# Kernel tuning notes

Hardware: AMD Instinct MI355X
Metric: run time of the kernel (lower is better)

The kernel has to match this reference:

```python
import jax, jax.numpy as jnp
import numpy as np

B, C, H, W = 8, 3, 1024, 1024
N, D, PS, NB, NH = 512, 256, 16, 8, 4


def _bin_matrix():
    # static radial-binning averaging matrix for a PS x (PS//2+1) rfft2 spectrum
    h, w = PS, PS // 2 + 1
    fy = np.fft.fftfreq(h)
    fx = np.linspace(0.0, 0.5, w)
    r = np.sqrt(fx[None, :] ** 2 + fy[:, None] ** 2)
    max_r = r.max() + 1e-6
    edges = np.linspace(0.0, max_r, NB + 1)
    idx = np.clip(np.searchsorted(edges, r.ravel(), side='right') - 1, 0, NB - 1)
    M = np.zeros((NB, h * w), np.float32)
    M[idx, np.arange(h * w)] = 1.0
    cnt = M.sum(1, keepdims=True)
    return M / np.maximum(cnt, 1.0)

_BIN_M = jnp.asarray(_bin_matrix())


def _ln(x, g, b, eps=1e-5):
    m = x.mean(-1, keepdims=True)
    v = x.var(-1, keepdims=True)
    return g * (x - m) / jnp.sqrt(v + eps) + b


def _gelu(x):
    return jax.nn.gelu(x, approximate=False)


def setup_inputs() -> dict:
    key = jax.random.key(0)
    ks = jax.random.split(key, 16)
    xav = lambda k, o, i: (jax.random.normal(k, (o, i)) / np.sqrt(i)).astype(jnp.float32)
    z = lambda n: jnp.zeros((n,), jnp.float32)
    o1 = lambda n: jnp.ones((n,), jnp.float32)
    FD = 2 * NB
    return {
        'image': jax.random.normal(ks[0], (B, C, H, W), jnp.float32),
        'point_coords': jax.random.uniform(ks[1], (B, N, 2), jnp.float32, 0.0, float(W)),
        'point_labels': jax.random.randint(ks[2], (B, N), 0, 2),
        'pe_w': xav(ks[3], D, D), 'pe_b': z(D),
        'type_emb': (0.02 * jax.random.normal(ks[4], (2, D))).astype(jnp.float32),
        'fbi': (1.0 + 0.1 * jax.random.normal(ks[5], (NB,))).astype(jnp.float32),
        'fe1_w': xav(ks[6], D // 2, FD), 'fe1_b': z(D // 2),
        'feln1_g': o1(D // 2), 'feln1_b': z(D // 2),
        'fe2_w': xav(ks[7], D, D // 2), 'fe2_b': z(D),
        'feln2_g': o1(D), 'feln2_b': z(D),
        'in_w': xav(ks[8], 3 * D, D), 'in_b': z(3 * D),
        'ao_w': xav(ks[9], D, D), 'ao_b': z(D),
        'n1_g': o1(D), 'n1_b': z(D),
        'f1_w': xav(ks[10], 2 * D, D), 'f1_b': z(2 * D),
        'f2_w': xav(ks[11], D, 2 * D), 'f2_b': z(D),
        'n2_g': o1(D), 'n2_b': z(D),
        'op_w': xav(ks[12], D, D), 'op_b': z(D),
    }


def reference(image, point_coords, point_labels, pe_w, pe_b, type_emb, fbi,
              fe1_w, fe1_b, feln1_g, feln1_b, fe2_w, fe2_b, feln2_g, feln2_b,
              in_w, in_b, ao_w, ao_b, n1_g, n1_b, f1_w, f1_b, f2_w, f2_b,
              n2_g, n2_b, op_w, op_b):
    Bv, Cv, Hv, Wv = image.shape
    Nv = point_coords.shape[1]
    # --- sinusoidal positional encoding (SAM style) + linear proj ---
    nc = point_coords / jnp.array([Wv, Hv], jnp.float32)
    dim_t = 10000.0 ** (2.0 * jnp.arange(D // 4, dtype=jnp.float32) / (D // 4))
    ax = (nc[..., 0:1] * (2.0 * np.pi)) / dim_t          # [B,N,D/4]
    ay = (nc[..., 1:2] * (2.0 * np.pi)) / dim_t
    pe = jnp.concatenate([jnp.sin(ax), jnp.cos(ax), jnp.sin(ay), jnp.cos(ay)], -1)
    spatial = pe @ pe_w.T + pe_b + type_emb[point_labels]  # [B,N,D]
    # --- batched per-point patch gather + rfft2 + radial binning ---
    gray = image.mean(1)                                   # [B,H,W]
    pc = jax.lax.stop_gradient(point_coords)               # .long() detaches in torch
    half = PS // 2
    px = jnp.clip(pc[..., 0].astype(jnp.int32), half, Wv - half - 1)
    py = jnp.clip(pc[..., 1].astype(jnp.int32), half, Hv - half - 1)
    off = jnp.arange(PS) - half
    rows = py[..., None] + off                             # [B,N,PS]
    cols = px[..., None] + off
    bidx = jnp.arange(Bv)[:, None, None, None]
    patches = gray[bidx, rows[..., :, None], cols[..., None, :]]  # [B,N,PS,PS]
    fft = jnp.fft.rfft2(patches, norm='ortho')             # [B,N,PS,PS//2+1]
    mag_bins = jnp.abs(fft).reshape(Bv, Nv, -1) @ _BIN_M.T    # [B,N,NB]
    ph_bins = jnp.angle(fft).reshape(Bv, Nv, -1) @ _BIN_M.T
    feat = jnp.concatenate([mag_bins * jax.nn.softmax(fbi), ph_bins], -1)  # [B,N,2*NB]
    # --- freq encoder MLP ---
    h1 = _gelu(_ln(feat @ fe1_w.T + fe1_b, feln1_g, feln1_b))
    freq = _ln(h1 @ fe2_w.T + fe2_b, feln2_g, feln2_b)     # [B,N,D]
    # --- cross-attention fusion (spatial = Q, freq = K/V) ---
    hd = D // NH
    q = (spatial @ in_w[:D].T + in_b[:D]).reshape(Bv, Nv, NH, hd)
    k = (freq @ in_w[D:2 * D].T + in_b[D:2 * D]).reshape(Bv, Nv, NH, hd)
    v = (freq @ in_w[2 * D:].T + in_b[2 * D:]).reshape(Bv, Nv, NH, hd)
    att = jax.nn.softmax(jnp.einsum('bqhd,bkhd->bhqk', q, k) / np.sqrt(hd), -1)
    o = jnp.einsum('bhqk,bkhd->bqhd', att, v).reshape(Bv, Nv, D)
    x = _ln(spatial + (o @ ao_w.T + ao_b), n1_g, n1_b)
    ffn = _gelu(x @ f1_w.T + f1_b) @ f2_w.T + f2_b
    x = _ln(x + ffn, n2_g, n2_b)
    return x @ op_w.T + op_b
```

## Files before the change

kernel.cpp:

```cpp
#include <hip/hip_runtime.h>
#include <math.h>


typedef __attribute__((ext_vector_type(8))) short short8;
typedef __attribute__((ext_vector_type(4))) float floatx4;
typedef unsigned short u16;
typedef unsigned long long u64;

__device__ __forceinline__ float gelu_f(float x) {
  return 0.5f * x * (1.0f + erff(x * 0.70710678118654752f));
}

__device__ __forceinline__ u16 bf16_rn(float x) {
  union { float f; unsigned u; } v; v.f = x;
  unsigned r = v.u + 0x7fffu + ((v.u >> 16) & 1u);
  return (u16)(r >> 16);
}

__device__ __forceinline__ void split_bf16(float x, u16& h, u16& l) {
  h = bf16_rn(x);
  union { unsigned u; float f; } hv; hv.u = ((unsigned)h) << 16;
  l = bf16_rn(x - hv.f);
}

#define W_PE   0
#define W_FE1  65536
#define W_FE2  67584
#define W_IN   100352
#define W_AO   296960
#define W_F1   362496
#define W_F2   493568
#define W_OP   624640


template <int NA, int K>
__device__ __forceinline__ void mm16_swz(
    const u16* Ah, const u16* Al, const int S,
    const u16* __restrict__ Bh, const u16* __restrict__ Bl,
    floatx4* acc)
{
  const int t = threadIdx.x;
  const int w = t >> 6, lane = t & 63;
  const int lm = lane & 15, kg = lane >> 4;
  #pragma unroll
  for (int it = 0; it < K / 32; ++it) {
    const short8 a_h = *(const short8*)&Ah[lm * S + it * 32 + kg * 8];
    const short8 a_l = *(const short8*)&Al[lm * S + it * 32 + kg * 8];
    #pragma unroll
    for (int nj = 0; nj < NA; nj++) {
      const size_t wo = (size_t)(((w * NA + nj) * (K / 32) + it) * 512 + lane * 8);
      const short8 b_h = *(const short8*)&Bh[wo];
      const short8 b_l = *(const short8*)&Bl[wo];
      acc[nj] = __builtin_amdgcn_mfma_f32_16x16x32_bf16(a_h, b_h, acc[nj], 0, 0, 0);
      acc[nj] = __builtin_amdgcn_mfma_f32_16x16x32_bf16(a_h, b_l, acc[nj], 0, 0, 0);
      acc[nj] = __builtin_amdgcn_mfma_f32_16x16x32_bf16(a_l, b_h, acc[nj], 0, 0, 0);
    }
  }
}

__device__ __forceinline__ void stage16(
    const u16* __restrict__ Gh, const u16* __restrict__ Gl,
    u16* Lh, u16* Ll)
{
  const int t = threadIdx.x;
  #pragma unroll
  for (int i = 0; i < 2; i++) {
    const int s = t + i * 256;
    const int row = s >> 5, c = (s & 31) * 8;
    *(short8*)&Lh[row * 264 + c] = *(const short8*)&Gh[(size_t)row * 256 + c];
    *(short8*)&Ll[row * 264 + c] = *(const short8*)&Gl[(size_t)row * 256 + c];
  }
  __syncthreads();
}

template <int N_, int NA>
__device__ __forceinline__ void ln_rows(const float (&v)[NA][4], float* red1, float* red2,
                                        float (&mean)[4], float (&rstd)[4])
{
  const int t = threadIdx.x;
  const int w = t >> 6;
  const int lane = t & 63;
  const int kg = lane >> 4;
  float s1[4] = {0.f,0.f,0.f,0.f}, s2[4] = {0.f,0.f,0.f,0.f};
  #pragma unroll
  for (int nj = 0; nj < NA; nj++)
    #pragma unroll
    for (int r = 0; r < 4; r++) { s1[r] += v[nj][r]; s2[r] += v[nj][r] * v[nj][r]; }
  #pragma unroll
  for (int r = 0; r < 4; r++) {
    #pragma unroll
    for (int off = 1; off < 16; off <<= 1) {
      s1[r] += __shfl_xor(s1[r], off);
      s2[r] += __shfl_xor(s2[r], off);
    }
  }
  __syncthreads();
  if ((lane & 15) == 0) {
    #pragma unroll
    for (int r = 0; r < 4; r++) {
      red1[w * 16 + kg * 4 + r] = s1[r];
      red2[w * 16 + kg * 4 + r] = s2[r];
    }
  }
  __syncthreads();
  #pragma unroll
  for (int r = 0; r < 4; r++) {
    const int rw = kg * 4 + r;
    const float a = red1[rw] + red1[16 + rw] + red1[32 + rw] + red1[48 + rw];
    const float b = red2[rw] + red2[16 + rw] + red2[32 + rw] + red2[48 + rw];
    mean[r] = a * (1.0f / N_);
    rstd[r] = rsqrtf(b * (1.0f / N_) - mean[r] * mean[r] + 1e-5f);
  }
}

__device__ __forceinline__ void store_swz(
    u16* __restrict__ Wh, u16* __restrict__ Wl, const int segbase,
    const int rel, const int kshift, const float4 v)
{
  const int K = 1 << kshift;
  const int n = rel >> kshift;
  const int k = rel & (K - 1);
  const int off8 = ((n >> 4) * (K >> 5) + (k >> 5)) * 512
                 + (((k >> 3) & 3) * 16 + (n & 15)) * 8 + (k & 7);
  u16 h0,h1,h2,h3,l0,l1,l2,l3;
  split_bf16(v.x,h0,l0); split_bf16(v.y,h1,l1);
  split_bf16(v.z,h2,l2); split_bf16(v.w,h3,l3);
  *(u64*)&Wh[segbase + off8] = (u64)h0 | ((u64)h1<<16) | ((u64)h2<<32) | ((u64)h3<<48);
  *(u64*)&Wl[segbase + off8] = (u64)l0 | ((u64)l1<<16) | ((u64)l2<<32) | ((u64)l3<<48);
}

__global__ __launch_bounds__(64) void k0_prep(
    const float* __restrict__ image, const float* __restrict__ coords,
    const float* __restrict__ fbi,
    const float* __restrict__ pe_w, const float* __restrict__ fe1_w,
    const float* __restrict__ fe2_w, const float* __restrict__ in_w,
    const float* __restrict__ ao_w, const float* __restrict__ f1_w,
    const float* __restrict__ f2_w, const float* __restrict__ op_w,
    u16* __restrict__ Wh, u16* __restrict__ Wl,
    u16* __restrict__ PEh, u16* __restrict__ PEl,
    u16* __restrict__ FEATh, u16* __restrict__ FEATl)
{
  const int blk = blockIdx.x;
  const int lane = threadIdx.x;

  if (blk < 2696) {
    const int idx = (blk * 64 + lane) * 4;
    if (idx < W_FE1) {
      store_swz(Wh, Wl, W_PE, idx - W_PE, 8, *(const float4*)&pe_w[idx - W_PE]);
    } else if (idx < W_FE2) {
      const int rel = idx - W_FE1;
      const float4 v = *(const float4*)&fe1_w[rel];
      u16 h0,h1,h2,h3,l0,l1,l2,l3;
      split_bf16(v.x,h0,l0); split_bf16(v.y,h1,l1);
      split_bf16(v.z,h2,l2); split_bf16(v.w,h3,l3);
      *(u64*)&Wh[idx] = (u64)h0 | ((u64)h1<<16) | ((u64)h2<<32) | ((u64)h3<<48);
      *(u64*)&Wl[idx] = (u64)l0 | ((u64)l1<<16) | ((u64)l2<<32) | ((u64)l3<<48);
    } else if (idx < W_IN) {
      store_swz(Wh, Wl, W_FE2, idx - W_FE2, 7, *(const float4*)&fe2_w[idx - W_FE2]);
    } else if (idx < W_AO) {
      store_swz(Wh, Wl, W_IN, idx - W_IN, 8, *(const float4*)&in_w[idx - W_IN]);
    } else if (idx < W_F1) {
      store_swz(Wh, Wl, W_AO, idx - W_AO, 8, *(const float4*)&ao_w[idx - W_AO]);
    } else if (idx < W_F2) {
      store_swz(Wh, Wl, W_F1, idx - W_F1, 8, *(const float4*)&f1_w[idx - W_F1]);
    } else if (idx < W_OP) {
      store_swz(Wh, Wl, W_F2, idx - W_F2, 9, *(const float4*)&f2_w[idx - W_F2]);
    } else {
      store_swz(Wh, Wl, W_OP, idx - W_OP, 8, *(const float4*)&op_w[idx - W_OP]);
    }
    return;
  }

  const int id = blk - 2696;
  const int b  = id >> 9;
  const float pcx = coords[id * 2 + 0];
  const float pcy = coords[id * 2 + 1];

  {
    const float TWO_PI = 6.283185307179586f;
    const float dimt = expf((float)lane * 0.28782313662425572f);
    const float ax = (pcx * (1.0f / 1024.0f)) * TWO_PI / dimt;
    const float ay = (pcy * (1.0f / 1024.0f)) * TWO_PI / dimt;
    u16 h, l;
    split_bf16(sinf(ax), h, l); PEh[id*256+lane]     = h; PEl[id*256+lane]     = l;
    split_bf16(cosf(ax), h, l); PEh[id*256+lane+64]  = h; PEl[id*256+lane+64]  = l;
    split_bf16(sinf(ay), h, l); PEh[id*256+lane+128] = h; PEl[id*256+lane+128] = l;
    split_bf16(cosf(ay), h, l); PEh[id*256+lane+192] = h; PEl[id*256+lane+192] = l;
  }

  int px = (int)pcx; px = px < 8 ? 8 : (px > 1015 ? 1015 : px);
  int py = (int)pcy; py = py < 8 ? 8 : (py > 1015 ? 1015 : py);

  __shared__ float patch[256];
  __shared__ float ct[16], st[16];
  __shared__ float Gre[144], Gim[144];
  __shared__ float msum[8], psum[8];
  __shared__ int cnt8[8];
  {
    const float* img = image + (size_t)b * 3145728;
    #pragma unroll
    for (int i = 0; i < 4; i++) {
      const int p = i * 64 + lane;
      const int r = p >> 4, c = p & 15;
      const int off = (py - 8 + r) * 1024 + (px - 8 + c);
      const float s = img[off] + img[off + 1048576] + img[off + 2097152];
      patch[r * 16 + c] = s * (1.0f / 3.0f);
    }
  }
  if (lane < 16) {
    float c, s;
    if ((lane & 3) == 0) {
      const float cv[4] = {1.0f, 0.0f, -1.0f, 0.0f};
      const float sv[4] = {0.0f, -1.0f, 0.0f, 1.0f};
      c = cv[lane >> 2]; s = sv[lane >> 2];
    } else {
      const float a = -3.14159265358979f * (float)lane * 0.125f;
      c = cosf(a); s = sinf(a);
    }
    ct[lane] = c; st[lane] = s;
  }
  if (lane < 8) { msum[lane] = 0.0f; psum[lane] = 0.0f; cnt8[lane] = 0; }
  __syncthreads();

  for (int tt = lane; tt < 144; tt += 64) {
    const int y = tt / 9, kx = tt - y * 9;
    float re = 0.0f, im = 0.0f;
    #pragma unroll
    for (int x = 0; x < 16; x++) {
      const int w = (x * kx) & 15;
      const float pv = patch[y * 16 + x];
      re = fmaf(pv, ct[w], re);
      im = fmaf(pv, st[w], im);
    }
    Gre[tt] = re; Gim[tt] = im;
  }
  __syncthreads();

  for (int tt = lane; tt < 144; tt += 64) {
    const int ky = tt / 9, kx = tt - ky * 9;
    float re = 0.0f, im = 0.0f;
    #pragma unroll
    for (int y = 0; y < 16; y++) {
      const int w = (y * ky) & 15;
      const float gr = Gre[y * 9 + kx], gi = Gim[y * 9 + kx];
      re = fmaf(gr, ct[w], re);
      re = fmaf(-gi, st[w], re);
      im = fmaf(gr, st[w], im);
      im = fmaf(gi, ct[w], im);
    }
    if (((ky & 7) == 0) && ((kx & 7) == 0)) im = 0.0f;
    const float mag = sqrtf(re * re + im * im) * 0.0625f;
    const float ph  = atan2f(im, re);

    const float fy = (ky < 8) ? (float)ky * 0.0625f : (float)(ky - 16) * 0.0625f;
    const float fx = (float)kx * 0.0625f;
    const float r = sqrtf(fx * fx + fy * fy);
    const float max_r = 0.7071077811865476f;
    const float stepf = max_r * 0.125f;
    int idx = 0;
    #pragma unroll
    for (int kq = 1; kq <= 8; kq++) {
      const float e = (kq == 8) ? max_r : stepf * (float)kq;
      if (r >= e) idx = kq;
    }
    if (idx > 7) idx = 7;
    atomicAdd(&msum[idx], mag);
    atomicAdd(&psum[idx], ph);
    atomicAdd(&cnt8[idx], 1);
  }
  __syncthreads();

  if (lane < 8) {
    float fm = fbi[0];
    #pragma unroll
    for (int j = 1; j < 8; j++) fm = fmaxf(fm, fbi[j]);
    float se = 0.0f;
    #pragma unroll
    for (int j = 0; j < 8; j++) se += expf(fbi[j] - fm);
    const float smx = expf(fbi[lane] - fm) / se;
    const float c = (float)(cnt8[lane] > 0 ? cnt8[lane] : 1);
    u16 h, l;
    split_bf16((msum[lane] / c) * smx, h, l);
    FEATh[id*16+lane] = h; FEATl[id*16+lane] = l;
    split_bf16(psum[lane] / c, h, l);
    FEATh[id*16+8+lane] = h; FEATl[id*16+8+lane] = l;
  }
}

__global__ __launch_bounds__(256) void k1_front(
    const u16* __restrict__ Wh, const u16* __restrict__ Wl,
    const u16* __restrict__ PEh, const u16* __restrict__ PEl,
    const u16* __restrict__ FEATh, const u16* __restrict__ FEATl,
    const float* __restrict__ pe_b, const int* __restrict__ labels,
    const float* __restrict__ temb,
    const float* __restrict__ fe1_b, const float* __restrict__ feln1_g, const float* __restrict__ feln1_b,
    const float* __restrict__ fe2_b, const float* __restrict__ feln2_g, const float* __restrict__ feln2_b,
    float* __restrict__ SPATIAL32, u16* __restrict__ SPh, u16* __restrict__ SPl,
    u16* __restrict__ FQh, u16* __restrict__ FQl)
{
  __shared__ __align__(16) u16 smem[8448];
  __shared__ float redbuf[128];
  const int blk = blockIdx.x;
  const int t = threadIdx.x;
  const int w = t >> 6, lane = t & 63;
  const int lm = lane & 15, kg = lane >> 4;

  if (blk < 256) {
    const int m0 = blk * 16;
    u16* Lh = smem;
    u16* Ll = smem + 4224;
    stage16(PEh + (size_t)m0 * 256, PEl + (size_t)m0 * 256, Lh, Ll);
    floatx4 acc[4];
    #pragma unroll
    for (int j = 0; j < 4; j++) acc[j] = (floatx4){0.f,0.f,0.f,0.f};
    mm16_swz<4, 256>(Lh, Ll, 264, Wh + W_PE, Wl + W_PE, acc);
    #pragma unroll
    for (int nj = 0; nj < 4; nj++) {
      const int col = w * 64 + nj * 16 + lm;
      #pragma unroll
      for (int r = 0; r < 4; r++) {
        const int row = m0 + kg * 4 + r;
        const float v = acc[nj][r] + pe_b[col] + temb[labels[row] * 256 + col];
        SPATIAL32[(size_t)row * 256 + col] = v;
        u16 h, l; split_bf16(v, h, l);
        SPh[(size_t)row * 256 + col] = h;
        SPl[(size_t)row * 256 + col] = l;
      }
    }
    return;
  }

  const int m0 = (blk - 256) * 16;
  u16* h1h = smem;
  u16* h1l = smem + 2176;

  floatx4 acc1[2];
  acc1[0] = (floatx4){0.f,0.f,0.f,0.f};
  acc1[1] = (floatx4){0.f,0.f,0.f,0.f};
  {
    const short8 zz = {0,0,0,0,0,0,0,0};
    const short8 a_h = (kg < 2) ? *(const short8*)&FEATh[(size_t)(m0 + lm) * 16 + kg * 8] : zz;
    const short8 a_l = (kg < 2) ? *(const short8*)&FEATl[(size_t)(m0 + lm) * 16 + kg * 8] : zz;
    #pragma unroll
    for (int nj = 0; nj < 2; nj++) {
      const int col = w * 32 + nj * 16 + lm;
      const short8 b_h = (kg < 2) ? *(const short8*)&Wh[W_FE1 + (size_t)col * 16 + kg * 8] : zz;
      const short8 b_l = (kg < 2) ? *(const short8*)&Wl[W_FE1 + (size_t)col * 16 + kg * 8] : zz;
      acc1[nj] = __builtin_amdgcn_mfma_f32_16x16x32_bf16(a_h, b_h, acc1[nj], 0, 0, 0);
      acc1[nj] = __builtin_amdgcn_mfma_f32_16x16x32_bf16(a_h, b_l, acc1[nj], 0, 0, 0);
      acc1[nj] = __builtin_amdgcn_mfma_f32_16x16x32_bf16(a_l, b_h, acc1[nj], 0, 0, 0);
    }
  }

  float v1[2][4];
  #pragma unroll
  for (int nj = 0; nj < 2; nj++) {
    const int col = w * 32 + nj * 16 + lm;
    #pragma unroll
    for (int r = 0; r < 4; r++) v1[nj][r] = acc1[nj][r] + fe1_b[col];
  }
  float mean[4], rstd[4];
  ln_rows<128, 2>(v1, redbuf, redbuf + 64, mean, rstd);
  #pragma unroll
  for (int nj = 0; nj < 2; nj++) {
    const int col = w * 32 + nj * 16 + lm;
    #pragma unroll
    for (int r = 0; r < 4; r++) {
      float y = feln1_g[col] * (v1[nj][r] - mean[r]) * rstd[r] + feln1_b[col];
      y = gelu_f(y);
      u16 h, l; split_bf16(y, h, l);
      h1h[(kg * 4 + r) * 136 + col] = h;
      h1l[(kg * 4 + r) * 136 + col] = l;
    }
  }
  __syncthreads();

  floatx4 acc2[4];
  #pragma unroll
  for (int j = 0; j < 4; j++) acc2[j] = (floatx4){0.f,0.f,0.f,0.f};
  mm16_swz<4, 128>(h1h, h1l, 136, Wh + W_FE2, Wl + W_FE2, acc2);

  float v2[4][4];
  #pragma unroll
  for (int nj = 0; nj < 4; nj++) {
    const int col = w * 64 + nj * 16 + lm;
    #pragma unroll
    for (int r = 0; r < 4; r++) v2[nj][r] = acc2[nj][r] + fe2_b[col];
  }
  ln_rows<256, 4>(v2, redbuf, redbuf + 64, mean, rstd);
  #pragma unroll
  for (int nj = 0; nj < 4; nj++) {
    const int col = w * 64 + nj * 16 + lm;
    #pragma unroll
    for (int r = 0; r < 4; r++) {
      const int rw = m0 + kg * 4 + r;
      float y = feln2_g[col] * (v2[nj][r] - mean[r]) * rstd[r] + feln2_b[col];
      u16 h, l; split_bf16(y, h, l);
      FQh[(size_t)rw * 256 + col] = h;
      FQl[(size_t)rw * 256 + col] = l;
    }
  }
}

__global__ __launch_bounds__(256) void k2_qkv(
    const u16* __restrict__ Wh, const u16* __restrict__ Wl,
    const u16* __restrict__ SPh, const u16* __restrict__ SPl,
    const u16* __restrict__ FQh, const u16* __restrict__ FQl,
    const float* __restrict__ in_b,
    u16* __restrict__ Qh, u16* __restrict__ Ql,
    u16* __restrict__ Kh, u16* __restrict__ Kl,
    u16* __restrict__ Vth, u16* __restrict__ Vtl)
{
  __shared__ __align__(16) u16 smem[8448];
  const int bx = blockIdx.x;
  const int seg = bx >> 8;
  const int m0 = (bx & 255) * 16;
  const int t = threadIdx.x;
  const int w = t >> 6, lane = t & 63;
  const int lm = lane & 15, kg = lane >> 4;

  const u16 *Ah, *Al; const u16 *Wsh, *Wsl; const float* bias;
  if (seg == 0)      { Ah = SPh; Al = SPl; Wsh = Wh + W_IN;          Wsl = Wl + W_IN;          bias = in_b; }
  else if (seg == 1) { Ah = FQh; Al = FQl; Wsh = Wh + W_IN + 65536;  Wsl = Wl + W_IN + 65536;  bias = in_b + 256; }
  else               { Ah = FQh; Al = FQl; Wsh = Wh + W_IN + 131072; Wsl = Wl + W_IN + 131072; bias = in_b + 512; }

  u16* Lh = smem;
  u16* Ll = smem + 4224;
  stage16(Ah + (size_t)m0 * 256, Al + (size_t)m0 * 256, Lh, Ll);

  floatx4 acc[4];
  #pragma unroll
  for (int j = 0; j < 4; j++) acc[j] = (floatx4){0.f,0.f,0.f,0.f};
  mm16_swz<4, 256>(Lh, Ll, 264, Wsh, Wsl, acc);

  if (seg < 2) {
    u16* oh = (seg == 0) ? Qh : Kh;
    u16* ol = (seg == 0) ? Ql : Kl;
    #pragma unroll
    for (int nj = 0; nj < 4; nj++) {
      const int col = w * 64 + nj * 16 + lm;
      #pragma unroll
      for (int r = 0; r < 4; r++) {
        const int row = m0 + kg * 4 + r;
        u16 h, l; split_bf16(acc[nj][r] + bias[col], h, l);
        oh[(size_t)row * 256 + col] = h;
        ol[(size_t)row * 256 + col] = l;
      }
    }
  } else {
    #pragma unroll
    for (int nj = 0; nj < 4; nj++) {
      const int col = w * 64 + nj * 16 + lm;
      u64 hp = 0, lp = 0;
      #pragma unroll
      for (int r = 0; r < 4; r++) {
        u16 h, l; split_bf16(acc[nj][r] + bias[col], h, l);
        hp |= ((u64)h) << (16 * r);
        lp |= ((u64)l) << (16 * r);
      }
      *(u64*)&Vth[(size_t)col * 4096 + m0 + kg * 4] = hp;
      *(u64*)&Vtl[(size_t)col * 4096 + m0 + kg * 4] = lp;
    }
  }
}

__global__ __launch_bounds__(256) void k3_attn(
    const u16* __restrict__ Qh, const u16* __restrict__ Ql,
    const u16* __restrict__ Kh, const u16* __restrict__ Kl,
    const u16* __restrict__ Vth, const u16* __restrict__ Vtl,
    u16* __restrict__ Oh, u16* __restrict__ Ol)
{
  __shared__ __align__(16) u16 smem[36864];
  u16* sQh = smem;
  u16* sQl = smem + 4608;
  u16* sKh = smem + 9216;
  u16* sKl = smem + 13824;
  u16* sVh = smem + 18432;
  u16* sVl = smem + 23040;
  u16* sPh = smem + 27648;
  u16* sPl = smem + 32256;

  const int qt = blockIdx.x & 7;
  const int bh = blockIdx.x >> 3;
  const int b = bh >> 2, h = bh & 3;
  const int t = threadIdx.x;
  const int w = t >> 6, lane = t & 63;
  const int lm = lane & 15, kg = lane >> 4;
  const int qrow0 = b * 512 + qt * 64;

  #pragma unroll
  for (int i = 0; i < 2; i++) {
    const int s = t + i * 256;
    const int r = s >> 3, d = (s & 7) * 8;
    *(short8*)&sQh[r * 72 + d] = *(const short8*)&Qh[(size_t)(qrow0 + r) * 256 + h * 64 + d];
    *(short8*)&sQl[r * 72 + d] = *(const short8*)&Ql[(size_t)(qrow0 + r) * 256 + h * 64 + d];
  }

  float m_i[4], l_i[4];
  floatx4 o_acc[4];
  #pragma unroll
  for (int r = 0; r < 4; r++) { m_i[r] = -INFINITY; l_i[r] = 0.0f; }
  #pragma unroll
  for (int dj = 0; dj < 4; dj++) o_acc[dj] = (floatx4){0.f, 0.f, 0.f, 0.f};

  __syncthreads();
  short8 q_h[2], q_l[2];
  #pragma unroll
  for (int ks = 0; ks < 2; ks++) {
    const int off = (w * 16 + lm) * 72 + ks * 32 + kg * 8;
    q_h[ks] = *(const short8*)&sQh[off];
    q_l[ks] = *(const short8*)&sQl[off];
  }

  for (int kt = 0; kt < 8; kt++) {
    __syncthreads();
    {
      const int krow0 = b * 512 + kt * 64;
      #pragma unroll
      for (int i = 0; i < 2; i++) {
        const int s = t + i * 256;
        const int r = s >> 3, d = (s & 7) * 8;
        *(short8*)&sKh[r * 72 + d] = *(const short8*)&Kh[(size_t)(krow0 + r) * 256 + h * 64 + d];
        *(short8*)&sKl[r * 72 + d] = *(const short8*)&Kl[(size_t)(krow0 + r) * 256 + h * 64 + d];
        *(short8*)&sVh[r * 72 + d] = *(const short8*)&Vth[(size_t)(h * 64 + r) * 4096 + krow0 + d];
        *(short8*)&sVl[r * 72 + d] = *(const short8*)&Vtl[(size_t)(h * 64 + r) * 4096 + krow0 + d];
      }
    }
    __syncthreads();

    floatx4 sacc[4];
    #pragma unroll
    for (int nj = 0; nj < 4; nj++) sacc[nj] = (floatx4){0.f, 0.f, 0.f, 0.f};
    #pragma unroll
    for (int ks = 0; ks < 2; ks++) {
      #pragma unroll
      for (int nj = 0; nj < 4; nj++) {
        const int off = (nj * 16 + lm) * 72 + ks * 32 + kg * 8;
        const short8 kb_h = *(const short8*)&sKh[off];
        const short8 kb_l = *(const short8*)&sKl[off];
        sacc[nj] = __builtin_amdgcn_mfma_f32_16x16x32_bf16(q_h[ks], kb_h, sacc[nj], 0, 0, 0);
        sacc[nj] = __builtin_amdgcn_mfma_f32_16x16x32_bf16(q_h[ks], kb_l, sacc[nj], 0, 0, 0);
        sacc[nj] = __builtin_amdgcn_mfma_f32_16x16x32_bf16(q_l[ks], kb_h, sacc[nj], 0, 0, 0);
      }
    }

    float pp[4][4];
    #pragma unroll
    for (int r = 0; r < 4; r++) {
      float mx = -INFINITY;
      #pragma unroll
      for (int nj = 0; nj < 4; nj++) {
        sacc[nj][r] *= 0.125f;
        mx = fmaxf(mx, sacc[nj][r]);
      }
      #pragma unroll
      for (int off = 1; off < 16; off <<= 1) mx = fmaxf(mx, __shfl_xor(mx, off));
      const float mnew = fmaxf(m_i[r], mx);
      const float alpha = expf(m_i[r] - mnew);
      m_i[r] = mnew;
      float rs = 0.0f;
      #pragma unroll
      for (int nj = 0; nj < 4; nj++) { pp[nj][r] = expf(sacc[nj][r] - mnew); rs += pp[nj][r]; }
      #pragma unroll
      for (int off = 1; off < 16; off <<= 1) rs += __shfl_xor(rs, off);
      l_i[r] = l_i[r] * alpha + rs;
      #pragma unroll
      for (int dj = 0; dj < 4; dj++) o_acc[dj][r] *= alpha;
    }

    #pragma unroll
    for (int nj = 0; nj < 4; nj++)
      #pragma unroll
      for (int r = 0; r < 4; r++) {
        u16 ph, pl; split_bf16(pp[nj][r], ph, pl);
        sPh[(w * 16 + kg * 4 + r) * 72 + nj * 16 + lm] = ph;
        sPl[(w * 16 + kg * 4 + r) * 72 + nj * 16 + lm] = pl;
      }

    #pragma unroll
    for (int ks = 0; ks < 2; ks++) {
      const short8 p_h = *(const short8*)&sPh[(w * 16 + lm) * 72 + ks * 32 + kg * 8];
      const short8 p_l = *(const short8*)&sPl[(w * 16 + lm) * 72 + ks * 32 + kg * 8];
      #pragma unroll
      for (int dj = 0; dj < 4; dj++) {
        const int off = (dj * 16 + lm) * 72 + ks * 32 + kg * 8;
        const short8 v_h = *(const short8*)&sVh[off];
        const short8 v_l = *(const short8*)&sVl[off];
        o_acc[dj] = __builtin_amdgcn_mfma_f32_16x16x32_bf16(p_h, v_h, o_acc[dj], 0, 0, 0);
        o_acc[dj] = __builtin_amdgcn_mfma_f32_16x16x32_bf16(p_l, v_h, o_acc[dj], 0, 0, 0);
        o_acc[dj] = __builtin_amdgcn_mfma_f32_16x16x32_bf16(p_h, v_l, o_acc[dj], 0, 0, 0);
      }
    }
  }

  #pragma unroll
  for (int r = 0; r < 4; r++) {
    const float inv_l = 1.0f / l_i[r];
    const size_t rowoff = (size_t)(qrow0 + w * 16 + kg * 4 + r) * 256 + h * 64;
    #pragma unroll
    for (int dj = 0; dj < 4; dj++) {
      u16 oh, ol; split_bf16(o_acc[dj][r] * inv_l, oh, ol);
      Oh[rowoff + dj * 16 + lm] = oh;
      Ol[rowoff + dj * 16 + lm] = ol;
    }
  }
}

__global__ __launch_bounds__(256) void k4_tail(
    const u16* __restrict__ Wh, const u16* __restrict__ Wl,
    const u16* __restrict__ Oh, const u16* __restrict__ Ol,
    const float* __restrict__ SPATIAL32,
    const float* __restrict__ ao_b, const float* __restrict__ n1_g, const float* __restrict__ n1_b,
    const float* __restrict__ f1_b, const float* __restrict__ f2_b,
    const float* __restrict__ n2_g, const float* __restrict__ n2_b,
    const float* __restrict__ op_b, float* __restrict__ OUT)
{
  __shared__ __align__(16) u16 smem[25088];
  __shared__ float redbuf[128];
  u16* B1h = smem;
  u16* B1l = smem + 4224;
  u16* Fh  = smem + 8448;
  u16* Fl  = smem + 16768;

  const int t = threadIdx.x;
  const int w = t >> 6, lane = t & 63;
  const int lm = lane & 15, kg = lane >> 4;
  const int m0 = blockIdx.x * 16;

  stage16(Oh + (size_t)m0 * 256, Ol + (size_t)m0 * 256, B1h, B1l);
  floatx4 acc[4];
  #pragma unroll
  for (int j = 0; j < 4; j++) acc[j] = (floatx4){0.f,0.f,0.f,0.f};
  mm16_swz<4, 256>(B1h, B1l, 264, Wh + W_AO, Wl + W_AO, acc);

  float x1reg[4][4];
  {
    float v[4][4];
    #pragma unroll
    for (int nj = 0; nj < 4; nj++) {
      const int col = w * 64 + nj * 16 + lm;
      #pragma unroll
      for (int r = 0; r < 4; r++)
        v[nj][r] = acc[nj][r] + ao_b[col] + SPATIAL32[(size_t)(m0 + kg * 4 + r) * 256 + col];
    }
    float mean[4], rstd[4];
    ln_rows<256, 4>(v, redbuf, redbuf + 64, mean, rstd);
    #pragma unroll
    for (int nj = 0; nj < 4; nj++) {
      const int col = w * 64 + nj * 16 + lm;
      #pragma unroll
      for (int r = 0; r < 4; r++) {
        const float y = n1_g[col] * (v[nj][r] - mean[r]) * rstd[r] + n1_b[col];
        x1reg[nj][r] = y;
        u16 h, l; split_bf16(y, h, l);
        B1h[(kg * 4 + r) * 264 + col] = h;
        B1l[(kg * 4 + r) * 264 + col] = l;
      }
    }
  }
  __syncthreads();

  #pragma unroll
  for (int ct = 0; ct < 2; ct++) {
    floatx4 a4[4];
    #pragma unroll
    for (int j = 0; j < 4; j++) a4[j] = (floatx4){0.f,0.f,0.f,0.f};
    mm16_swz<4, 256>(B1h, B1l, 264,
                     Wh + W_F1 + (size_t)ct * 65536, Wl + W_F1 + (size_t)ct * 65536, a4);
    #pragma unroll
    for (int nj = 0; nj < 4; nj++) {
      const int col = ct * 256 + w * 64 + nj * 16 + lm;
      #pragma unroll
      for (int r = 0; r < 4; r++) {
        const float y = gelu_f(a4[nj][r] + f1_b[col]);
        u16 h, l; split_bf16(y, h, l);
        Fh[(kg * 4 + r) * 520 + col] = h;
        Fl[(kg * 4 + r) * 520 + col] = l;
      }
    }
  }
  __syncthreads();

  #pragma unroll
  for (int j = 0; j < 4; j++) acc[j] = (floatx4){0.f,0.f,0.f,0.f};
  mm16_swz<4, 512>(Fh, Fl, 520, Wh + W_F2, Wl + W_F2, acc);
  {
    float v[4][4];
    #pragma unroll
    for (int nj = 0; nj < 4; nj++) {
      const int col = w * 64 + nj * 16 + lm;
      #pragma unroll
      for (int r = 0; r < 4; r++)
        v[nj][r] = acc[nj][r] + f2_b[col] + x1reg[nj][r];
    }
    float mean[4], rstd[4];
    ln_rows<256, 4>(v, redbuf, redbuf + 64, mean, rstd);
    #pragma unroll
    for (int nj = 0; nj < 4; nj++) {
      const int col = w * 64 + nj * 16 + lm;
      #pragma unroll
      for (int r = 0; r < 4; r++) {
        const float y = n2_g[col] * (v[nj][r] - mean[r]) * rstd[r] + n2_b[col];
        u16 h, l; split_bf16(y, h, l);
        B1h[(kg * 4 + r) * 264 + col] = h;
        B1l[(kg * 4 + r) * 264 + col] = l;
      }
    }
  }
  __syncthreads();

  #pragma unroll
  for (int j = 0; j < 4; j++) acc[j] = (floatx4){0.f,0.f,0.f,0.f};
  mm16_swz<4, 256>(B1h, B1l, 264, Wh + W_OP, Wl + W_OP, acc);
  #pragma unroll
  for (int nj = 0; nj < 4; nj++) {
    const int col = w * 64 + nj * 16 + lm;
    #pragma unroll
    for (int r = 0; r < 4; r++)
      OUT[(size_t)(m0 + kg * 4 + r) * 256 + col] = acc[nj][r] + op_b[col];
  }
}

extern "C" void kernel_launch(void* const* d_in, const int* in_sizes, int n_in,
                              void* d_out, int out_size, void* d_ws, size_t ws_size,
                              hipStream_t stream) {
  const float* image   = (const float*)d_in[0];
  const float* coords  = (const float*)d_in[1];
  const int*   labels  = (const int*)d_in[2];
  const float* pe_w    = (const float*)d_in[3];
  const float* pe_b    = (const float*)d_in[4];
  const float* temb    = (const float*)d_in[5];
  const float* fbi     = (const float*)d_in[6];
  const float* fe1_w   = (const float*)d_in[7];
  const float* fe1_b   = (const float*)d_in[8];
  const float* feln1_g = (const float*)d_in[9];
  const float* feln1_b = (const float*)d_in[10];
  const float* fe2_w   = (const float*)d_in[11];
  const float* fe2_b   = (const float*)d_in[12];
  const float* feln2_g = (const float*)d_in[13];
  const float* feln2_b = (const float*)d_in[14];
  const float* in_w    = (const float*)d_in[15];
  const float* in_b    = (const float*)d_in[16];
  const float* ao_w    = (const float*)d_in[17];
  const float* ao_b    = (const float*)d_in[18];
  const float* n1_g    = (const float*)d_in[19];
  const float* n1_b    = (const float*)d_in[20];
  const float* f1_w    = (const float*)d_in[21];
  const float* f1_b    = (const float*)d_in[22];
  const float* f2_w    = (const float*)d_in[23];
  const float* f2_b    = (const float*)d_in[24];
  const float* n2_g    = (const float*)d_in[25];
  const float* n2_b    = (const float*)d_in[26];
  const float* op_w    = (const float*)d_in[27];
  const float* op_b    = (const float*)d_in[28];

  float* ws = (float*)d_ws;
  float* SPATIAL32 = ws;
  u16* S = (u16*)(ws + 2 * (1u << 20));
  u16* Wh = S;
  u16* Wl = S + 690176;
  u16* PEh   = S + 1380352;  u16* PEl   = PEh + 1048576;
  u16* FEATh = S + 3477504;  u16* FEATl = FEATh + 65536;
  u16* FQh   = S + 4657152;  u16* FQl   = FQh + 1048576;
  u16* SPh   = S + 6754304;  u16* SPl   = SPh + 1048576;
  u16* Qh    = S + 8851456;  u16* Ql    = Qh + 1048576;
  u16* Kh    = S + 10948608; u16* Kl    = Kh + 1048576;
  u16* Vth   = S + 13045760; u16* Vtl   = Vth + 1048576;
  u16* Oh    = S + 15142912; u16* Ol    = Oh + 1048576;

  float* OUT = (float*)d_out;

  k0_prep<<<6792, 64, 0, stream>>>(
      image, coords, fbi, pe_w, fe1_w, fe2_w, in_w, ao_w, f1_w, f2_w, op_w,
      Wh, Wl, PEh, PEl, FEATh, FEATl);
  k1_front<<<512, 256, 0, stream>>>(
      Wh, Wl, PEh, PEl, FEATh, FEATl, pe_b, labels, temb,
      fe1_b, feln1_g, feln1_b, fe2_b, feln2_g, feln2_b,
      SPATIAL32, SPh, SPl, FQh, FQl);
  k2_qkv<<<768, 256, 0, stream>>>(
      Wh, Wl, SPh, SPl, FQh, FQl, in_b, Qh, Ql, Kh, Kl, Vth, Vtl);
  k3_attn<<<256, 256, 0, stream>>>(Qh, Ql, Kh, Kl, Vth, Vtl, Oh, Ol);
  k4_tail<<<256, 256, 0, stream>>>(
      Wh, Wl, Oh, Ol, SPATIAL32, ao_b, n1_g, n1_b, f1_b, f2_b, n2_g, n2_b, op_b, OUT);
}
```

Measured before the change: 315.3 us.

## Split-K across extra waves in attention and tail kernels

The attention kernel now runs 512 threads per block, with two wave sets each covering half of the key tiles. Their flash-attention partial states (max, sum, output) are merged through shared memory at the end. The tail kernel runs 1024 threads, with four wave sets splitting the K dimension of every GEMM and reducing partial sums in shared memory before the layernorm and activation epilogues. The aim is more parallelism per block, since only 256 blocks fill the GPU, at the cost of extra syncs, more LDS use and idle waves during epilogues.

```diff
diff --git a/kernel.cpp b/kernel.cpp
--- a/kernel.cpp
+++ b/kernel.cpp
@@ -58,6 +58,65 @@
   }
 }
 
+template <int NA, int K>
+__device__ __forceinline__ void mm16_ks(
+    const u16* Ah, const u16* Al, const int S,
+    const u16* __restrict__ Bh, const u16* __restrict__ Bl,
+    floatx4* acc)
+{
+  const int t = threadIdx.x;
+  const int w = t >> 6, lane = t & 63;
+  const int ww = w & 3, set = w >> 2;
+  const int lm = lane & 15, kg = lane >> 4;
+  #pragma unroll
+  for (int itl = 0; itl < K / 128; ++itl) {
+    const int it = set * (K / 128) + itl;
+    const short8 a_h = *(const short8*)&Ah[lm * S + it * 32 + kg * 8];
+    const short8 a_l = *(const short8*)&Al[lm * S + it * 32 + kg * 8];
+    #pragma unroll
+    for (int nj = 0; nj < NA; nj++) {
+      const size_t wo = (size_t)(((ww * NA + nj) * (K / 32) + it) * 512 + lane * 8);
+      const short8 b_h = *(const short8*)&Bh[wo];
+      const short8 b_l = *(const short8*)&Bl[wo];
+      acc[nj] = __builtin_amdgcn_mfma_f32_16x16x32_bf16(a_h, b_h, acc[nj], 0, 0, 0);
+      acc[nj] = __builtin_amdgcn_mfma_f32_16x16x32_bf16(a_h, b_l, acc[nj], 0, 0, 0);
+      acc[nj] = __builtin_amdgcn_mfma_f32_16x16x32_bf16(a_l, b_h, acc[nj], 0, 0, 0);
+    }
+  }
+}
+
+template <int NA>
+__device__ __forceinline__ void reduce_sets(floatx4* acc, float* PART)
+{
+  const int t = threadIdx.x;
+  const int w = t >> 6, lane = t & 63;
+  const int ww = w & 3, set = w >> 2;
+  const int lm = lane & 15, kg = lane >> 4;
+  __syncthreads();
+  if (set != 0) {
+    #pragma unroll
+    for (int nj = 0; nj < NA; nj++) {
+      const int col = ww * (NA * 16) + nj * 16 + lm;
+      #pragma unroll
+      for (int r = 0; r < 4; r++)
+        PART[((set - 1) * 16 + kg * 4 + r) * 260 + col] = acc[nj][r];
+    }
+  }
+  __syncthreads();
+  if (set == 0) {
+    #pragma unroll
+    for (int nj = 0; nj < NA; nj++) {
+      const int col = ww * (NA * 16) + nj * 16 + lm;
+      #pragma unroll
+      for (int r = 0; r < 4; r++) {
+        const int rr = kg * 4 + r;
+        acc[nj][r] += PART[rr * 260 + col] + PART[(16 + rr) * 260 + col]
+                    + PART[(32 + rr) * 260 + col];
+      }
+    }
+  }
+}
+
 __device__ __forceinline__ void stage16(
     const u16* __restrict__ Gh, const u16* __restrict__ Gl,
     u16* Lh, u16* Ll)
@@ -110,6 +169,49 @@
     const float b = red2[rw] + red2[16 + rw] + red2[32 + rw] + red2[48 + rw];
     mean[r] = a * (1.0f / N_);
     rstd[r] = rsqrtf(b * (1.0f / N_) - mean[r] * mean[r] + 1e-5f);
+  }
+}
+
+template <int N_, int NA>
+__device__ __forceinline__ void ln_rows16(const float (&v)[NA][4], float* red1, float* red2,
+                                          float (&mean)[4], float (&rstd)[4])
+{
+  const int t = threadIdx.x;
+  const int w = t >> 6;
+  const int lane = t & 63;
+  const int ww = w & 3, set = w >> 2;
+  const int kg = lane >> 4;
+  float s1[4] = {0.f,0.f,0.f,0.f}, s2[4] = {0.f,0.f,0.f,0.f};
+  #pragma unroll
+  for (int nj = 0; nj < NA; nj++)
+    #pragma unroll
+    for (int r = 0; r < 4; r++) { s1[r] += v[nj][r]; s2[r] += v[nj][r] * v[nj][r]; }
+  #pragma unroll
+  for (int r = 0; r < 4; r++) {
+    #pragma unroll
+    for (int off = 1; off < 16; off <<= 1) {
+      s1[r] += __shfl_xor(s1[r], off);
+      s2[r] += __shfl_xor(s2[r], off);
+    }
+  }
+  __syncthreads();
+  if (set == 0 && (lane & 15) == 0) {
+    #pragma unroll
+    for (int r = 0; r < 4; r++) {
+      red1[ww * 16 + kg * 4 + r] = s1[r];
+      red2[ww * 16 + kg * 4 + r] = s2[r];
+    }
+  }
+  __syncthreads();
+  if (set == 0) {
+    #pragma unroll
+    for (int r = 0; r < 4; r++) {
+      const int rw = kg * 4 + r;
+      const float a = red1[rw] + red1[16 + rw] + red1[32 + rw] + red1[48 + rw];
+      const float b = red2[rw] + red2[16 + rw] + red2[32 + rw] + red2[48 + rw];
+      mean[r] = a * (1.0f / N_);
+      rstd[r] = rsqrtf(b * (1.0f / N_) - mean[r] * mean[r] + 1e-5f);
+    }
   }
 }
 
@@ -464,34 +566,38 @@
   }
 }
 
-__global__ __launch_bounds__(256) void k3_attn(
+__global__ __launch_bounds__(512) void k3_attn(
     const u16* __restrict__ Qh, const u16* __restrict__ Ql,
     const u16* __restrict__ Kh, const u16* __restrict__ Kl,
     const u16* __restrict__ Vth, const u16* __restrict__ Vtl,
     u16* __restrict__ Oh, u16* __restrict__ Ol)
 {
-  __shared__ __align__(16) u16 smem[36864];
+  __shared__ __align__(16) u16 smem[64512];
+  __shared__ float O1[64 * 68];
+  __shared__ float Mbuf[64], Lbuf[64];
+
+  const int t = threadIdx.x;
+  const int w = t >> 6, lane = t & 63;
+  const int ww = w & 3, set = w >> 2;
+  const int lm = lane & 15, kg = lane >> 4;
+  const int ts = t & 255;
+
   u16* sQh = smem;
   u16* sQl = smem + 4608;
-  u16* sKh = smem + 9216;
-  u16* sKl = smem + 13824;
-  u16* sVh = smem + 18432;
-  u16* sVl = smem + 23040;
-  u16* sPh = smem + 27648;
-  u16* sPl = smem + 32256;
+  u16* sKh = smem + 9216 + set * 27648;
+  u16* sKl = sKh + 4608;
+  u16* sVh = sKh + 9216;
+  u16* sVl = sKh + 13824;
+  u16* sPh = sKh + 18432;
+  u16* sPl = sKh + 23040;
 
   const int qt = blockIdx.x & 7;
   const int bh = blockIdx.x >> 3;
   const int b = bh >> 2, h = bh & 3;
-  const int t = threadIdx.x;
-  const int w = t >> 6, lane = t & 63;
-  const int lm = lane & 15, kg = lane >> 4;
   const int qrow0 = b * 512 + qt * 64;
 
-  #pragma unroll
-  for (int i = 0; i < 2; i++) {
-    const int s = t + i * 256;
-    const int r = s >> 3, d = (s & 7) * 8;
+  {
+    const int r = t >> 3, d = (t & 7) * 8;
     *(short8*)&sQh[r * 72 + d] = *(const short8*)&Qh[(size_t)(qrow0 + r) * 256 + h * 64 + d];
     *(short8*)&sQl[r * 72 + d] = *(const short8*)&Ql[(size_t)(qrow0 + r) * 256 + h * 64 + d];
   }
@@ -507,18 +613,19 @@
   short8 q_h[2], q_l[2];
   #pragma unroll
   for (int ks = 0; ks < 2; ks++) {
-    const int off = (w * 16 + lm) * 72 + ks * 32 + kg * 8;
+    const int off = (ww * 16 + lm) * 72 + ks * 32 + kg * 8;
     q_h[ks] = *(const short8*)&sQh[off];
     q_l[ks] = *(const short8*)&sQl[off];
   }
 
-  for (int kt = 0; kt < 8; kt++) {
+  for (int ktl = 0; ktl < 4; ktl++) {
+    const int kt = set * 4 + ktl;
     __syncthreads();
     {
       const int krow0 = b * 512 + kt * 64;
       #pragma unroll
       for (int i = 0; i < 2; i++) {
-        const int s = t + i * 256;
+        const int s = ts + i * 256;
         const int r = s >> 3, d = (s & 7) * 8;
         *(short8*)&sKh[r * 72 + d] = *(const short8*)&Kh[(size_t)(krow0 + r) * 256 + h * 64 + d];
         *(short8*)&sKl[r * 72 + d] = *(const short8*)&Kl[(size_t)(krow0 + r) * 256 + h * 64 + d];
@@ -573,14 +680,14 @@
       #pragma unroll
       for (int r = 0; r < 4; r++) {
         u16 ph, pl; split_bf16(pp[nj][r], ph, pl);
-        sPh[(w * 16 + kg * 4 + r) * 72 + nj * 16 + lm] = ph;
-        sPl[(w * 16 + kg * 4 + r) * 72 + nj * 16 + lm] = pl;
+        sPh[(ww * 16 + kg * 4 + r) * 72 + nj * 16 + lm] = ph;
+        sPl[(ww * 16 + kg * 4 + r) * 72 + nj * 16 + lm] = pl;
       }
 
     #pragma unroll
     for (int ks = 0; ks < 2; ks++) {
-      const short8 p_h = *(const short8*)&sPh[(w * 16 + lm) * 72 + ks * 32 + kg * 8];
-      const short8 p_l = *(const short8*)&sPl[(w * 16 + lm) * 72 + ks * 32 + kg * 8];
+      const short8 p_h = *(const short8*)&sPh[(ww * 16 + lm) * 72 + ks * 32 + kg * 8];
+      const short8 p_l = *(const short8*)&sPl[(ww * 16 + lm) * 72 + ks * 32 + kg * 8];
       #pragma unroll
       for (int dj = 0; dj < 4; dj++) {
         const int off = (dj * 16 + lm) * 72 + ks * 32 + kg * 8;
@@ -593,20 +700,39 @@
     }
   }
 
-  #pragma unroll
-  for (int r = 0; r < 4; r++) {
-    const float inv_l = 1.0f / l_i[r];
-    const size_t rowoff = (size_t)(qrow0 + w * 16 + kg * 4 + r) * 256 + h * 64;
-    #pragma unroll
-    for (int dj = 0; dj < 4; dj++) {
-      u16 oh, ol; split_bf16(o_acc[dj][r] * inv_l, oh, ol);
-      Oh[rowoff + dj * 16 + lm] = oh;
-      Ol[rowoff + dj * 16 + lm] = ol;
-    }
-  }
-}
-
-__global__ __launch_bounds__(256) void k4_tail(
+  if (set == 1) {
+    #pragma unroll
+    for (int r = 0; r < 4; r++) {
+      const int row = ww * 16 + kg * 4 + r;
+      if (lm == 0) { Mbuf[row] = m_i[r]; Lbuf[row] = l_i[r]; }
+      #pragma unroll
+      for (int dj = 0; dj < 4; dj++)
+        O1[row * 68 + dj * 16 + lm] = o_acc[dj][r];
+    }
+  }
+  __syncthreads();
+  if (set == 0) {
+    #pragma unroll
+    for (int r = 0; r < 4; r++) {
+      const int row = ww * 16 + kg * 4 + r;
+      const float m1 = Mbuf[row], l1v = Lbuf[row];
+      const float mnew = fmaxf(m_i[r], m1);
+      const float a0 = expf(m_i[r] - mnew);
+      const float a1 = expf(m1 - mnew);
+      const float inv_l = 1.0f / (l_i[r] * a0 + l1v * a1);
+      const size_t rowoff = (size_t)(qrow0 + row) * 256 + h * 64;
+      #pragma unroll
+      for (int dj = 0; dj < 4; dj++) {
+        const float val = (o_acc[dj][r] * a0 + O1[row * 68 + dj * 16 + lm] * a1) * inv_l;
+        u16 hh, ll; split_bf16(val, hh, ll);
+        Oh[rowoff + dj * 16 + lm] = hh;
+        Ol[rowoff + dj * 16 + lm] = ll;
+      }
+    }
+  }
+}
+
+__global__ __launch_bounds__(1024) void k4_tail(
     const u16* __restrict__ Wh, const u16* __restrict__ Wl,
     const u16* __restrict__ Oh, const u16* __restrict__ Ol,
     const float* __restrict__ SPATIAL32,
@@ -617,6 +743,7 @@
 {
   __shared__ __align__(16) u16 smem[25088];
   __shared__ float redbuf[128];
+  __shared__ float PART[3 * 16 * 260];
   u16* B1h = smem;
   u16* B1l = smem + 4224;
   u16* Fh  = smem + 8448;
@@ -624,37 +751,58 @@
 
   const int t = threadIdx.x;
   const int w = t >> 6, lane = t & 63;
+  const int ww = w & 3, set = w >> 2;
   const int lm = lane & 15, kg = lane >> 4;
   const int m0 = blockIdx.x * 16;
 
-  stage16(Oh + (size_t)m0 * 256, Ol + (size_t)m0 * 256, B1h, B1l);
+  {
+    const u16* Gh = Oh + (size_t)m0 * 256;
+    const u16* Gl = Ol + (size_t)m0 * 256;
+    if (t < 512) {
+      const int row = t >> 5, c = (t & 31) * 8;
+      *(short8*)&B1h[row * 264 + c] = *(const short8*)&Gh[(size_t)row * 256 + c];
+      *(short8*)&B1l[row * 264 + c] = *(const short8*)&Gl[(size_t)row * 256 + c];
+    }
+    __syncthreads();
+  }
+
   floatx4 acc[4];
   #pragma unroll
   for (int j = 0; j < 4; j++) acc[j] = (floatx4){0.f,0.f,0.f,0.f};
-  mm16_swz<4, 256>(B1h, B1l, 264, Wh + W_AO, Wl + W_AO, acc);
+  mm16_ks<4, 256>(B1h, B1l, 264, Wh + W_AO, Wl + W_AO, acc);
+  reduce_sets<4>(acc, PART);
 
   float x1reg[4][4];
   {
     float v[4][4];
-    #pragma unroll
-    for (int nj = 0; nj < 4; nj++) {
-      const int col = w * 64 + nj * 16 + lm;
-      #pragma unroll
-      for (int r = 0; r < 4; r++)
-        v[nj][r] = acc[nj][r] + ao_b[col] + SPATIAL32[(size_t)(m0 + kg * 4 + r) * 256 + col];
+    if (set == 0) {
+      #pragma unroll
+      for (int nj = 0; nj < 4; nj++) {
+        const int col = ww * 64 + nj * 16 + lm;
+        #pragma unroll
+        for (int r = 0; r < 4; r++)
+          v[nj][r] = acc[nj][r] + ao_b[col] + SPATIAL32[(size_t)(m0 + kg * 4 + r) * 256 + col];
+      }
+    } else {
+      #pragma unroll
+      for (int nj = 0; nj < 4; nj++)
+        #pragma unroll
+        for (int r = 0; r < 4; r++) v[nj][r] = 0.0f;
     }
     float mean[4], rstd[4];
-    ln_rows<256, 4>(v, redbuf, redbuf + 64, mean, rstd);
-    #pragma unroll
-    for (int nj = 0; nj < 4; nj++) {
-      const int col = w * 64 + nj * 16 + lm;
-      #pragma unroll
-      for (int r = 0; r < 4; r++) {
-        const float y = n1_g[col] * (v[nj][r] - mean[r]) * rstd[r] + n1_b[col];
-        x1reg[nj][r] = y;
-        u16 h, l; split_bf16(y, h, l);
-        B1h[(kg * 4 + r) * 264 + col] = h;
-        B1l[(kg * 4 + r) * 264 + col] = l;
+    ln_rows16<256, 4>(v, redbuf, redbuf + 64, mean, rstd);
+    if (set == 0) {
+      #pragma unroll
+      for (int nj = 0; nj < 4; nj++) {
+        const int col = ww * 64 + nj * 16 + lm;
+        #pragma unroll
+        for (int r = 0; r < 4; r++) {
+          const float y = n1_g[col] * (v[nj][r] - mean[r]) * rstd[r] + n1_b[col];
+          x1reg[nj][r] = y;
+          u16 h, l; split_bf16(y, h, l);
+          B1h[(kg * 4 + r) * 264 + col] = h;
+          B1l[(kg * 4 + r) * 264 + col] = l;
+        }
       }
     }
   }
@@ -665,17 +813,20 @@
     floatx4 a4[4];
     #pragma unroll
     for (int j = 0; j < 4; j++) a4[j] = (floatx4){0.f,0.f,0.f,0.f};
-    mm16_swz<4, 256>(B1h, B1l, 264,
-                     Wh + W_F1 + (size_t)ct * 65536, Wl + W_F1 + (size_t)ct * 65536, a4);
-    #pragma unroll
-    for (int nj = 0; nj < 4; nj++) {
-      const int col = ct * 256 + w * 64 + nj * 16 + lm;
-      #pragma unroll
-      for (int r = 0; r < 4; r++) {
-        const float y = gelu_f(a4[nj][r] + f1_b[col]);
-        u16 h, l; split_bf16(y, h, l);
-        Fh[(kg * 4 + r) * 520 + col] = h;
-        Fl[(kg * 4 + r) * 520 + col] = l;
+    mm16_ks<4, 256>(B1h, B1l, 264,
+                    Wh + W_F1 + (size_t)ct * 65536, Wl + W_F1 + (size_t)ct * 65536, a4);
+    reduce_sets<4>(a4, PART);
+    if (set == 0) {
+      #pragma unroll
+      for (int nj = 0; nj < 4; nj++) {
+        const int col = ct * 256 + ww * 64 + nj * 16 + lm;
+        #pragma unroll
+        for (int r = 0; r < 4; r++) {
+          const float y = gelu_f(a4[nj][r] + f1_b[col]);
+          u16 h, l; split_bf16(y, h, l);
+          Fh[(kg * 4 + r) * 520 + col] = h;
+          Fl[(kg * 4 + r) * 520 + col] = l;
+        }
       }
     }
   }
@@ -683,41 +834,54 @@
 
   #pragma unroll
   for (int j = 0; j < 4; j++) acc[j] = (floatx4){0.f,0.f,0.f,0.f};
-  mm16_swz<4, 512>(Fh, Fl, 520, Wh + W_F2, Wl + W_F2, acc);
+  mm16_ks<4, 512>(Fh, Fl, 520, Wh + W_F2, Wl + W_F2, acc);
+  reduce_sets<4>(acc, PART);
   {
     float v[4][4];
+    if (set == 0) {
+      #pragma unroll
+      for (int nj = 0; nj < 4; nj++) {
+        const int col = ww * 64 + nj * 16 + lm;
+        #pragma unroll
+        for (int r = 0; r < 4; r++)
+          v[nj][r] = acc[nj][r] + f2_b[col] + x1reg[nj][r];
+      }
+    } else {
+      #pragma unroll
+      for (int nj = 0; nj < 4; nj++)
+        #pragma unroll
+        for (int r = 0; r < 4; r++) v[nj][r] = 0.0f;
+    }
+    float mean[4], rstd[4];
+    ln_rows16<256, 4>(v, redbuf, redbuf + 64, mean, rstd);
+    if (set == 0) {
+      #pragma unroll
+      for (int nj = 0; nj < 4; nj++) {
+        const int col = ww * 64 + nj * 16 + lm;
+        #pragma unroll
+        for (int r = 0; r < 4; r++) {
+          const float y = n2_g[col] * (v[nj][r] - mean[r]) * rstd[r] + n2_b[col];
+          u16 h, l; split_bf16(y, h, l);
+          B1h[(kg * 4 + r) * 264 + col] = h;
+          B1l[(kg * 4 + r) * 264 + col] = l;
+        }
+      }
+    }
+  }
+  __syncthreads();
+
+  #pragma unroll
+  for (int j = 0; j < 4; j++) acc[j] = (floatx4){0.f,0.f,0.f,0.f};
+  mm16_ks<4, 256>(B1h, B1l, 264, Wh + W_OP, Wl + W_OP, acc);
+  reduce_sets<4>(acc, PART);
+  if (set == 0) {
     #pragma unroll
     for (int nj = 0; nj < 4; nj++) {
-      const int col = w * 64 + nj * 16 + lm;
+      const int col = ww * 64 + nj * 16 + lm;
       #pragma unroll
       for (int r = 0; r < 4; r++)
-        v[nj][r] = acc[nj][r] + f2_b[col] + x1reg[nj][r];
-    }
-    float mean[4], rstd[4];
-    ln_rows<256, 4>(v, redbuf, redbuf + 64, mean, rstd);
-    #pragma unroll
-    for (int nj = 0; nj < 4; nj++) {
-      const int col = w * 64 + nj * 16 + lm;
-      #pragma unroll
-      for (int r = 0; r < 4; r++) {
-        const float y = n2_g[col] * (v[nj][r] - mean[r]) * rstd[r] + n2_b[col];
-        u16 h, l; split_bf16(y, h, l);
-        B1h[(kg * 4 + r) * 264 + col] = h;
-        B1l[(kg * 4 + r) * 264 + col] = l;
-      }
-    }
-  }
-  __syncthreads();
-
-  #pragma unroll
-  for (int j = 0; j < 4; j++) acc[j] = (floatx4){0.f,0.f,0.f,0.f};
-  mm16_swz<4, 256>(B1h, B1l, 264, Wh + W_OP, Wl + W_OP, acc);
-  #pragma unroll
-  for (int nj = 0; nj < 4; nj++) {
-    const int col = w * 64 + nj * 16 + lm;
-    #pragma unroll
-    for (int r = 0; r < 4; r++)
-      OUT[(size_t)(m0 + kg * 4 + r) * 256 + col] = acc[nj][r] + op_b[col];
+        OUT[(size_t)(m0 + kg * 4 + r) * 256 + col] = acc[nj][r] + op_b[col];
+    }
   }
 }
 
@@ -779,7 +943,7 @@
       SPATIAL32, SPh, SPl, FQh, FQl);
   k2_qkv<<<768, 256, 0, stream>>>(
       Wh, Wl, SPh, SPl, FQh, FQl, in_b, Qh, Ql, Kh, Kl, Vth, Vtl);
-  k3_attn<<<256, 256, 0, stream>>>(Qh, Ql, Kh, Kl, Vth, Vtl, Oh, Ol);
-  k4_tail<<<256, 256, 0, stream>>>(
+  k3_attn<<<256, 512, 0, stream>>>(Qh, Ql, Kh, Kl, Vth, Vtl, Oh, Ol);
+  k4_tail<<<256, 1024, 0, stream>>>(
       Wh, Wl, Oh, Ol, SPATIAL32, ao_b, n1_g, n1_b, f1_b, f2_b, n2_g, n2_b, op_b, OUT);
 }
```

Measured after the change: 287.1 us. -9.0%, faster.
